# Kernel optimization log

Measured on AMD Instinct MI355X. Metric: run time of the kernel, lower is better.

The kernel has to match this reference:

```python
import jax, jax.numpy as jnp
import numpy as np

H = 400      # LSTM hidden units
K = 10       # attention window mixture components (mixtures=30 -> alpha/beta/kappa of size K)
V = 61       # vocab_size
NOUT = 121   # MDN head: 1 eos + 20*(pi, mu1, mu2, sigma1, sigma2, rho)


def setup_inputs():
    key = jax.random.key(0)
    ks = jax.random.split(key, 12)
    B, T, U = 32, 600, 64
    s = 0.05
    d = {}
    d['strokes'] = jax.random.normal(ks[0], (B, T, 3), jnp.float32)
    d['sentence'] = jax.random.uniform(ks[1], (B, U, V), dtype=jnp.float32)
    d['W1'] = jax.random.normal(ks[2], (3 + V, 4 * H), jnp.float32) * s
    d['U1r'] = jax.random.normal(ks[3], (H, 4 * H), jnp.float32) * s
    d['b1'] = jnp.zeros((4 * H,), jnp.float32)
    d['Ww'] = jax.random.normal(ks[4], (H, 3 * K), jnp.float32) * s
    d['bw'] = jnp.zeros((3 * K,), jnp.float32)
    d['W2'] = jax.random.normal(ks[5], (3 + V + H, 4 * H), jnp.float32) * s
    d['U2r'] = jax.random.normal(ks[6], (H, 4 * H), jnp.float32) * s
    d['b2'] = jnp.zeros((4 * H,), jnp.float32)
    d['W3'] = jax.random.normal(ks[7], (3 + V + H, 4 * H), jnp.float32) * s
    d['U3r'] = jax.random.normal(ks[8], (H, 4 * H), jnp.float32) * s
    d['b3'] = jnp.zeros((4 * H,), jnp.float32)
    d['Wm'] = jax.random.normal(ks[9], (3 * H, NOUT), jnp.float32) * s
    d['bm'] = jnp.zeros((NOUT,), jnp.float32)
    return d


def _lstm(x_tbd, W, Ur, b, h0, c0):
    # standard Keras-order (i, f, g, o) LSTM over time-major input [T,B,D]
    def step(carry, xt):
        h, c = carry
        z = xt @ W + h @ Ur + b
        i, f, g, o = jnp.split(z, 4, axis=-1)
        c = jax.nn.sigmoid(f) * c + jax.nn.sigmoid(i) * jnp.tanh(g)
        h = jax.nn.sigmoid(o) * jnp.tanh(c)
        return (h, c), h
    _, hs = jax.lax.scan(step, (h0, c0), x_tbd)
    return hs


def _forward(strokes, sentence, W1, U1r, b1, Ww, bw, W2, U2r, b2, W3, U3r, b3, Wm, bm):
    B, T, _ = strokes.shape
    U = sentence.shape[1]
    u_grid = jnp.arange(U, dtype=strokes.dtype)           # character positions
    x_tb = jnp.transpose(strokes, (1, 0, 2))               # [T,B,3]
    h0 = jnp.zeros((B, H), strokes.dtype)
    w0 = jnp.zeros((B, V), strokes.dtype)
    k0 = jnp.zeros((B, K), strokes.dtype)

    def step1(carry, xt):
        # Graves synthesis windowed LSTM cell: LSTM on [x_t, w_{t-1}],
        # then Gaussian-mixture soft attention over the sentence.
        h, c, w, kappa = carry
        xin = jnp.concatenate([xt, w], axis=-1)            # [B, 3+V]
        z = xin @ W1 + h @ U1r + b1
        i, f, g, o = jnp.split(z, 4, axis=-1)
        c = jax.nn.sigmoid(f) * c + jax.nn.sigmoid(i) * jnp.tanh(g)
        h = jax.nn.sigmoid(o) * jnp.tanh(c)
        p = h @ Ww + bw                                    # [B, 3K]
        alpha = jnp.exp(p[:, :K])
        beta = jnp.exp(p[:, K:2 * K])
        kappa = kappa + jnp.exp(p[:, 2 * K:])
        # phi(u) = sum_k alpha_k exp(-beta_k (kappa_k - u)^2)  -> [B,U]
        phi = jnp.einsum('bk,bku->bu', alpha,
                         jnp.exp(-beta[:, :, None] * (kappa[:, :, None] - u_grid) ** 2))
        w = jnp.einsum('bu,buv->bv', phi, sentence)        # soft window [B,V]
        return (h, c, w, kappa), jnp.concatenate([h, w], axis=-1)

    _, o1 = jax.lax.scan(step1, (h0, h0, w0, k0), x_tb)    # [T,B,H+V]
    lstm1 = o1[:, :, :H]
    win = o1[:, :, H:]
    in2 = jnp.concatenate([x_tb, win, lstm1], axis=-1)     # skip1: [T,B,3+V+H]
    lstm2 = _lstm(in2, W2, U2r, b2, h0, h0)
    in3 = jnp.concatenate([x_tb, win, lstm2], axis=-1)     # skip2
    lstm3 = _lstm(in3, W3, U3r, b3, h0, h0)
    y = jnp.concatenate([lstm1, lstm2, lstm3], axis=-1) @ Wm + bm  # [T,B,121]
    # MDN mixture coefficients
    e = jax.nn.sigmoid(y[..., 0:1])
    pi = jax.nn.softmax(y[..., 1:21], axis=-1)
    mu1 = y[..., 21:41]
    mu2 = y[..., 41:61]
    s1 = jnp.exp(y[..., 61:81])
    s2 = jnp.exp(y[..., 81:101])
    rho = jnp.tanh(y[..., 101:121])
    out = jnp.concatenate([e, pi, mu1, mu2, s1, s2, rho], axis=-1)
    return jnp.transpose(out, (1, 0, 2))                   # [B,T,121]


def reference(strokes, sentence, W1, U1r, b1, Ww, bw, W2, U2r, b2, W3, U3r, b3, Wm, bm):
    return _forward(strokes, sentence, W1, U1r, b1, Ww, bw, W2, U2r, b2, W3, U3r, b3, Wm, bm)
```

## Files before the change

### kernel.cpp

```cpp
#include <hip/hip_runtime.h>
#include <math.h>

#define T 600
#define NBLK 235

#define SEN1 256
#define SEN2 384
#define SEN3 512
#define SENB 640

#define OFF_UT1 8192
#define SZ_UT1 (1600*480)
#define OFF_UT2 (OFF_UT1 + SZ_UT1)
#define SZ_UT2 (1600*960)
#define OFF_UT3 (OFF_UT2 + SZ_UT2)
#define OFF_WWT (OFF_UT3 + SZ_UT2)
#define SZ_WWT (30*400)
#define OFF_H1 (OFF_WWT + SZ_WWT)
#define SZ_H (600*32*400)
#define OFF_H2 (OFF_H1 + SZ_H)
#define OFF_H3 (OFF_H2 + SZ_H)
#define OFF_W  (OFF_H3 + SZ_H)
#define SZ_W (600*32*61)

#define LDS_W    0
#define LDS_V    19280
#define LDS_Z    34640
#define LDS_C    35408
#define LDS_TOT  35600

__device__ __forceinline__ float sigm(float x) { return 1.f/(1.f+expf(-x)); }

#define WBAR() do { \
    asm volatile("s_waitcnt lgkmcnt(0)" ::: "memory"); \
    __builtin_amdgcn_sched_barrier(0); \
} while (0)

__global__ void init_ws(unsigned* uws) {
    for (int i = threadIdx.x + blockIdx.x*blockDim.x; i < 8192; i += blockDim.x*gridDim.x)
        uws[i] = 0u;
}

__global__ void build_ut(float* __restrict__ ws,
                         const float* __restrict__ W1, const float* __restrict__ U1r,
                         const float* __restrict__ W2, const float* __restrict__ U2r,
                         const float* __restrict__ W3, const float* __restrict__ U3r,
                         const float* __restrict__ Ww) {
    const long N1 = 1600L*480, N2 = 1600L*960;
    const long total = N1 + 2*N2 + 30L*400;
    for (long i = blockIdx.x*(long)blockDim.x + threadIdx.x; i < total;
         i += (long)gridDim.x*blockDim.x) {
        if (i < N1) {
            long c = i / 480, k = i % 480;
            float v = 0.f;
            if (k < 64) v = W1[k*1600 + c];
            else if (k < 464) v = U1r[(k-64)*1600 + c];
            ws[OFF_UT1 + c*480 + k] = v;
        } else if (i < N1 + N2) {
            long ii = i - N1; long c = ii/960, k = ii%960;
            float v = 0.f;
            if (k < 464) v = W2[k*1600 + c];
            else if (k >= 480 && k < 880) v = U2r[(k-480)*1600 + c];
            ws[OFF_UT2 + c*960 + k] = v;
        } else if (i < N1 + 2*N2) {
            long ii = i - N1 - N2; long c = ii/960, k = ii%960;
            float v = 0.f;
            if (k < 464) v = W3[k*1600 + c];
            else if (k >= 480 && k < 880) v = U3r[(k-480)*1600 + c];
            ws[OFF_UT3 + c*960 + k] = v;
        } else {
            long ii = i - N1 - 2*N2; long n = ii/400, k = ii%400;
            ws[OFF_WWT + n*400 + k] = Ww[k*30 + n];
        }
    }
}

__device__ __forceinline__ unsigned ld_cohere(const unsigned* p) {
    unsigned v;
    asm volatile("global_load_dword %0, %1, off sc0 sc1\n\t"
                 "s_waitcnt vmcnt(0)"
                 : "=v"(v) : "v"(p) : "memory");
    return v;
}
__device__ __forceinline__ void st_wt(float* p, float v) {
    asm volatile("global_store_dword %0, %1, off sc0 sc1\n\t"
                 "s_waitcnt vmcnt(0)"
                 :: "v"(p), "v"(v) : "memory");
}
__device__ __forceinline__ void st_wt_u(unsigned* p, unsigned v) {
    asm volatile("global_store_dword %0, %1, off sc0 sc1\n\t"
                 "s_waitcnt vmcnt(0)"
                 :: "v"(p), "v"(v) : "memory");
}
__device__ __forceinline__ void wait_sen(const unsigned* sen, int count,
                                         unsigned tgt, int tid) {
    if (tid < 64) {
        for (;;) {
            unsigned m = 0xFFFFFFFFu;
            for (int i = tid; i < count; i += 64) {
                unsigned v = ld_cohere(sen + i);
                m = (v < m) ? v : m;
            }
            if (__all(m >= tgt)) break;
            __builtin_amdgcn_s_sleep(1);
        }
    }
    __syncthreads();
}

template<int NQ, int KCN, int K4S, int LO, int HI>
__device__ __forceinline__ void gemm_pass(const float4* __restrict__ w4,
                                          const float4* __restrict__ v4,
                                          int lc0, int kc, int bq, int kofs4,
                                          float acc[8][4]) {
    #pragma unroll
    for (int q = 0; q < NQ; ++q) {
        int kfv = q*KCN + kc;
        if (kfv >= LO && kfv < HI) {
            int xv = kfv ^ ((kfv >> 3) & 7);
            int kfw = kofs4 + kfv;
            int xw = kfw ^ ((kfw >> 3) & 7);
            float4 va[8];
            #pragma unroll
            for (int i = 0; i < 8; ++i) va[i] = v4[(bq*8+i)*120 + xv];
            #pragma unroll
            for (int j = 0; j < 4; ++j) {
                float4 u = w4[(lc0+j)*K4S + xw];
                #pragma unroll
                for (int i = 0; i < 8; ++i)
                    acc[i][j] += va[i].x*u.x + va[i].y*u.y + va[i].z*u.z + va[i].w*u.w;
            }
        }
    }
}

__launch_bounds__(512)
__global__ void hw_main(float* __restrict__ ws,
                        const float* __restrict__ strokes, const float* __restrict__ sentence,
                        const float* __restrict__ b1, const float* __restrict__ b2,
                        const float* __restrict__ b3, const float* __restrict__ bw) {
    extern __shared__ float S[];
    const int tid = threadIdx.x;
    const int bid = blockIdx.x;
    unsigned* uws = (unsigned*)ws;
    const unsigned* sen1 = uws + SEN1;
    const unsigned* sen2 = uws + SEN2;
    const unsigned* sen3 = uws + SEN3;
    const unsigned* senB = uws + SENB;

    int role, unit0 = 0, nu = 0, L = 0, b0a = 0;
    const float* utp = nullptr; const float* biasp = nullptr; float* hout = nullptr;
    if (bid < 67)       { role = 0; L = bid;      unit0 = L*6; nu = (bid==66)?4:6; utp = ws+OFF_UT1; biasp = b1; hout = ws+OFF_H1; }
    else if (bid < 147) { role = 1; L = bid-67;   unit0 = L*5; nu = 5;             utp = ws+OFF_UT2; biasp = b2; hout = ws+OFF_H2; }
    else if (bid < 227) { role = 2; L = bid-147;  unit0 = L*5; nu = 5;             utp = ws+OFF_UT3; biasp = b3; hout = ws+OFF_H3; }
    else                { role = 3; L = bid-227;  b0a = L*4; }

    if (role <= 2) {
        const int NC = 4*nu;
        const int KCN = (role == 0) ? 20 : 24;
        const int K4S = (role == 0) ? 121 : 241;
        const int K4TOT = (role == 0) ? 120 : 240;
        const int uts = (role == 0) ? 480 : 960;
        float4* w4 = (float4*)S;
        float4* v4 = (float4*)(S + LDS_V);
        float*  vf = S + LDS_V;
        float*  z_lds = S + LDS_Z;
        float*  c_lds = S + LDS_C;

        for (int idx = tid; idx < NC*K4TOT; idx += 512) {
            int colL = idx / K4TOT, kf = idx % K4TOT;
            int gcol = (colL/nu)*400 + unit0 + (colL%nu);
            float4 val = *(const float4*)(utp + (size_t)gcol*uts + kf*4);
            w4[colL*K4S + (kf ^ ((kf>>3)&7))] = val;
        }
        for (int i = tid; i < 192; i += 512) c_lds[i] = 0.f;

        const int tile = tid / KCN, kc = tid % KCN;
        const int bq = tile / nu, cq = tile % nu;
        const bool act = (tile < 4*nu);
        float bias0 = 0.f, bias1 = 0.f;
        if (tid < 32*NC)       { int lc = tid % NC;        bias0 = biasp[(lc/nu)*400 + unit0 + (lc%nu)]; }
        if (tid + 512 < 32*NC) { int lc = (tid+512) % NC;  bias1 = biasp[(lc/nu)*400 + unit0 + (lc%nu)]; }
        const int nrole = (role == 0) ? 67 : 80;
        const unsigned* mysen = (role == 0) ? sen1 : ((role == 1) ? sen2 : sen3);
        unsigned* myword = (unsigned*)mysen + L;
        __syncthreads();

        for (int t = 0; t < T; ++t) {
            float acc[8][4];
            #pragma unroll
            for (int i = 0; i < 8; ++i)
                #pragma unroll
                for (int j = 0; j < 4; ++j) acc[i][j] = 0.f;

            if (role == 0) {
                if (t > 0) wait_sen(sen1, 67, (unsigned)t, tid);
                const float* hsrc = (t > 0) ? (ws + OFF_H1 + (size_t)(t-1)*12800) : nullptr;
                for (int idx = tid; idx < 3328; idx += 512) {
                    int b = idx/104, kf = 16 + idx%104;
                    float4 val = {0.f,0.f,0.f,0.f};
                    if (kf < 116 && hsrc) val = *(const float4*)(hsrc + b*400 + (kf*4 - 64));
                    v4[b*120 + (kf ^ ((kf>>3)&7))] = val;
                }
                __syncthreads();
                if (act) gemm_pass<6,20,121,16,116>(w4, v4, cq*4, kc, bq, 0, acc);
                if (t > 0) wait_sen(senB, 8, (unsigned)t, tid);
                const float* wsrc = (t > 0) ? (ws + OFF_W + (size_t)(t-1)*1952) : nullptr;
                {
                    int b = tid / 16, kf = tid % 16;
                    if (b < 32) {
                        float4 val;
                        if (kf == 0) {
                            const float* xp = strokes + ((size_t)b*600 + t)*3;
                            val.x = xp[0]; val.y = xp[1]; val.z = xp[2];
                            val.w = wsrc ? wsrc[b*61] : 0.f;
                        } else {
                            int k0 = kf*4 - 3;
                            if (wsrc) { val.x = wsrc[b*61+k0]; val.y = wsrc[b*61+k0+1];
                                        val.z = wsrc[b*61+k0+2]; val.w = wsrc[b*61+k0+3]; }
                            else { val.x=val.y=val.z=val.w=0.f; }
                        }
                        v4[b*120 + (kf ^ ((kf>>3)&7))] = val;
                    }
                }
                __syncthreads();
                if (act) gemm_pass<6,20,121,0,16>(w4, v4, cq*4, kc, bq, 0, acc);
            } else {
                if (role == 1) wait_sen(senB, 8, (unsigned)(t+1), tid);
                else           wait_sen(sen2, 80, (unsigned)(t+1), tid);
                const float* hsrc = ws + ((role==1)?OFF_H1:OFF_H2) + (size_t)t*12800;
                const float* wsrc = ws + OFF_W + (size_t)t*1952;
                for (int idx = tid; idx < 3840; idx += 512) {
                    int b = idx/120, kf = idx%120;
                    float4 val;
                    if (kf >= 16) {
                        if (kf < 116) val = *(const float4*)(hsrc + b*400 + (kf*4 - 64));
                        else { val.x=val.y=val.z=val.w=0.f; }
                    } else if (kf == 0) {
                        const float* xp = strokes + ((size_t)b*600 + t)*3;
                        val.x = xp[0]; val.y = xp[1]; val.z = xp[2];
                        val.w = wsrc[b*61];
                    } else {
                        int k0 = kf*4 - 3;
                        val.x = wsrc[b*61+k0]; val.y = wsrc[b*61+k0+1];
                        val.z = wsrc[b*61+k0+2]; val.w = wsrc[b*61+k0+3];
                    }
                    v4[b*120 + (kf ^ ((kf>>3)&7))] = val;
                }
                __syncthreads();
                if (act) gemm_pass<5,24,241,0,116>(w4, v4, cq*4, kc, bq, 0, acc);
                __syncthreads();
                if (t > 0) wait_sen(mysen, 80, (unsigned)t, tid);
                const float* hp2 = (t > 0) ? (ws + ((role==1)?OFF_H2:OFF_H3) + (size_t)(t-1)*12800) : nullptr;
                for (int idx = tid; idx < 3840; idx += 512) {
                    int b = idx/120, kf = idx%120;
                    float4 val = {0.f,0.f,0.f,0.f};
                    if (kf < 100 && hp2) val = *(const float4*)(hp2 + b*400 + kf*4);
                    v4[b*120 + (kf ^ ((kf>>3)&7))] = val;
                }
                __syncthreads();
                if (act) gemm_pass<5,24,241,0,100>(w4, v4, cq*4, kc, bq, 120, acc);
            }

            __syncthreads();
            const int halfk = (KCN+1)/2;
            const int SCRW = NC*32 + 4;
            const int NO = 32*NC;
            if (act && kc < halfk) {
                #pragma unroll
                for (int i = 0; i < 8; ++i) {
                    float4 w;
                    w.x=acc[i][0]; w.y=acc[i][1]; w.z=acc[i][2]; w.w=acc[i][3];
                    *(float4*)&vf[kc*SCRW + (bq*8+i)*NC + cq*4] = w;
                }
            }
            __syncthreads();
            float zs0 = 0.f, zs1 = 0.f;
            if (tid < NO)       for (int k2 = 0; k2 < halfk; ++k2) zs0 += vf[k2*SCRW + tid];
            if (tid + 512 < NO) for (int k2 = 0; k2 < halfk; ++k2) zs1 += vf[k2*SCRW + tid + 512];
            __syncthreads();
            if (act && kc >= halfk) {
                #pragma unroll
                for (int i = 0; i < 8; ++i) {
                    float4 w;
                    w.x=acc[i][0]; w.y=acc[i][1]; w.z=acc[i][2]; w.w=acc[i][3];
                    *(float4*)&vf[(kc-halfk)*SCRW + (bq*8+i)*NC + cq*4] = w;
                }
            }
            __syncthreads();
            const int rem = KCN - halfk;
            if (tid < NO) {
                for (int k2 = 0; k2 < rem; ++k2) zs0 += vf[k2*SCRW + tid];
                z_lds[tid] = zs0 + bias0;
            }
            if (tid + 512 < NO) {
                for (int k2 = 0; k2 < rem; ++k2) zs1 += vf[k2*SCRW + tid + 512];
                z_lds[tid + 512] = zs1 + bias1;
            }
            __syncthreads();
            if (tid < 32*nu) {
                int b = tid & 31, ju = tid >> 5;
                float zi = z_lds[b*NC + ju];
                float zf = z_lds[b*NC + nu + ju];
                float zg = z_lds[b*NC + 2*nu + ju];
                float zo = z_lds[b*NC + 3*nu + ju];
                float cP = c_lds[b*6 + ju];
                float cN = sigm(zf)*cP + sigm(zi)*tanhf(zg);
                float hN = sigm(zo)*tanhf(cN);
                c_lds[b*6 + ju] = cN;
                st_wt(&hout[(size_t)t*12800 + b*400 + unit0 + ju], hN);
            }
            __syncthreads();
            if (tid == 0) st_wt_u(myword, (unsigned)(t+1));
        }
    } else {
        const int wv = tid >> 6, lane = tid & 63;
        float* hb   = S;
        float* pb   = S + 1600 + (tid>>6)*32;
        float* ab   = S + 1792 + (tid>>6)*32;
        float* kap  = S + 1984 + (tid>>6)*16;
        float* phiW = S + 2112 + (tid>>6)*64;
        float* sentl= S + 2368;
        float* wwt  = S + 2368 + 15616;
        float* hbW  = hb + wv*400;
        float4* hb4 = (float4*)hbW;
        unsigned* myword = (unsigned*)senB + L;

        for (int i = tid; i < 64; i += 512) (S + 1984)[i] = 0.f;
        for (int i = tid; i < 15616; i += 512) sentl[i] = sentence[(size_t)b0a*3904 + i];
        for (int i = tid; i < 12000; i += 512) {
            int n = i/400, k = i%400;
            wwt[n*404 + k] = ws[OFF_WWT + i];
        }
        float bwv = (lane < 60 && !(lane & 1)) ? bw[lane >> 1] : 0.f;
        __syncthreads();

        for (int t = 0; t < T; ++t) {
            wait_sen(sen1, 67, (unsigned)(t+1), tid);
            if (wv < 4) {
                const float* h1t = ws + OFF_H1 + (size_t)t*12800 + (size_t)(b0a+wv)*400;
                for (int i = lane; i < 100; i += 64)
                    hb4[i] = *(const float4*)(h1t + i*4);
                WBAR();
                if (lane < 60) {
                    int n = lane >> 1, hf = lane & 1;
                    const float4* ww4 = (const float4*)(wwt + n*404) + hf*50;
                    const float4* hh4 = hb4 + hf*50;
                    float a = 0.f;
                    #pragma unroll 5
                    for (int i = 0; i < 50; ++i) {
                        float4 h = hh4[i], w = ww4[i];
                        a += h.x*w.x + h.y*w.y + h.z*w.z + h.w*w.w;
                    }
                    a += __shfl_xor(a, 1);
                    if (hf == 0) pb[n] = a + bwv;
                }
                WBAR();
                if (lane < 10) {
                    ab[lane]      = expf(pb[lane]);
                    ab[16 + lane] = expf(pb[10 + lane]);
                    kap[lane]    += expf(pb[20 + lane]);
                }
                WBAR();
                {
                    float uf = (float)lane, ph = 0.f;
                    #pragma unroll
                    for (int k0 = 0; k0 < 10; ++k0) {
                        float d = kap[k0] - uf;
                        ph += ab[k0]*expf(-ab[16 + k0]*d*d);
                    }
                    phiW[lane] = ph;
                }
                WBAR();
                if (lane < 61) {
                    const float* sp = sentl + wv*3904 + lane;
                    float wvv = 0.f;
                    #pragma unroll 4
                    for (int u = 0; u < 64; ++u) wvv += phiW[u]*sp[u*61];
                    st_wt(&ws[OFF_W + (size_t)t*1952 + (size_t)(b0a+wv)*61 + lane], wvv);
                }
            }
            __syncthreads();
            if (tid == 0) st_wt_u(myword, (unsigned)(t+1));
        }
    }
}

__launch_bounds__(256)
__global__ void out_proj(const float* __restrict__ ws, const float* __restrict__ Wm,
                         const float* __restrict__ bm, float* __restrict__ out) {
    __shared__ __align__(16) float hc[8*1200];
    __shared__ float yy[8*121];
    __shared__ float sm2[16];
    const int tid = threadIdx.x;
    const long rowbase = (long)blockIdx.x * 8;
    const float* h1h = ws + OFF_H1;
    const float* h2h = ws + OFF_H2;
    const float* h3h = ws + OFF_H3;
    for (int idx = tid; idx < 8*1200; idx += 256) {
        int i = idx/1200, k = idx%1200;
        long r = rowbase + i; int t = (int)(r >> 5), b = (int)(r & 31);
        float v;
        if (k < 400)      v = h1h[(size_t)t*12800 + b*400 + k];
        else if (k < 800) v = h2h[(size_t)t*12800 + b*400 + (k-400)];
        else              v = h3h[(size_t)t*12800 + b*400 + (k-800)];
        hc[i*1200 + k] = v;
    }
    __syncthreads();
    const int j = tid & 127, rr = tid >> 7;
    if (j < 121) {
        float a0=0.f, a1=0.f, a2=0.f, a3=0.f;
        const float* r0 = &hc[(rr*4+0)*1200];
        const float* r1 = &hc[(rr*4+1)*1200];
        const float* r2 = &hc[(rr*4+2)*1200];
        const float* r3 = &hc[(rr*4+3)*1200];
        for (int k = 0; k < 1200; ++k) {
            float wm = Wm[(size_t)k*121 + j];
            a0 += r0[k]*wm; a1 += r1[k]*wm; a2 += r2[k]*wm; a3 += r3[k]*wm;
        }
        float bb = bm[j];
        yy[(rr*4+0)*121 + j] = a0 + bb;
        yy[(rr*4+1)*121 + j] = a1 + bb;
        yy[(rr*4+2)*121 + j] = a2 + bb;
        yy[(rr*4+3)*121 + j] = a3 + bb;
    }
    __syncthreads();
    if (tid < 8) {
        const float* yr = &yy[tid*121];
        float m = yr[1];
        for (int q = 2; q < 21; ++q) m = fmaxf(m, yr[q]);
        float ssum = 0.f;
        for (int q = 1; q < 21; ++q) ssum += expf(yr[q] - m);
        sm2[tid*2] = m; sm2[tid*2+1] = ssum;
    }
    __syncthreads();
    if (j < 121) {
        for (int i2 = 0; i2 < 4; ++i2) {
            int i = rr*4 + i2;
            long r = rowbase + i; int t = (int)(r >> 5), b = (int)(r & 31);
            float y = yy[i*121 + j], o;
            if (j == 0)      o = 1.f/(1.f + expf(-y));
            else if (j < 21) o = expf(y - sm2[i*2]) / sm2[i*2+1];
            else if (j < 61) o = y;
            else if (j < 101) o = expf(y);
            else             o = tanhf(y);
            out[((size_t)b*600 + t)*121 + j] = o;
        }
    }
}

extern "C" void kernel_launch(void* const* d_in, const int* in_sizes, int n_in,
                              void* d_out, int out_size, void* d_ws, size_t ws_size,
                              hipStream_t stream) {
    const float* strokes  = (const float*)d_in[0];
    const float* sentence = (const float*)d_in[1];
    const float* W1  = (const float*)d_in[2];
    const float* U1r = (const float*)d_in[3];
    const float* b1  = (const float*)d_in[4];
    const float* Ww  = (const float*)d_in[5];
    const float* bw  = (const float*)d_in[6];
    const float* W2  = (const float*)d_in[7];
    const float* U2r = (const float*)d_in[8];
    const float* b2  = (const float*)d_in[9];
    const float* W3  = (const float*)d_in[10];
    const float* U3r = (const float*)d_in[11];
    const float* b3  = (const float*)d_in[12];
    const float* Wm  = (const float*)d_in[13];
    const float* bm  = (const float*)d_in[14];
    float* ws = (float*)d_ws;
    float* out = (float*)d_out;

    const int dyn_bytes = LDS_TOT * 4;
    (void)hipFuncSetAttribute((const void*)hw_main,
                              hipFuncAttributeMaxDynamicSharedMemorySize, dyn_bytes);

    init_ws<<<dim3(4), dim3(512), 0, stream>>>((unsigned*)ws);
    build_ut<<<dim3(1024), dim3(256), 0, stream>>>(ws, W1, U1r, W2, U2r, W3, U3r, Ww);
    hw_main<<<dim3(NBLK), dim3(512), dyn_bytes, stream>>>(ws, strokes, sentence, b1, b2, b3, bw);
    out_proj<<<dim3(2400), dim3(256), 0, stream>>>(ws, Wm, bm, out);
}
```

Measured before the change: 10.51 ms.

## Defer window/stroke input contribution of layer-1 LSTM until after the recurrent GEMM reduction

Layer-1 LSTM blocks no longer wait for the attention window before their second GEMM pass. They first run the recurrent h-part GEMM and its reduction, then wait for the window signal. The x and window contribution (64 inputs) is then computed as a small per-thread dot product against a head weight slice cached in LDS, fused into the gate nonlinearity. The aim is to take the window-block dependency off the critical path of the GEMM, at the cost of a serial 64-term dot product per output thread and extra LDS.

```diff
diff --git a/kernel.cpp b/kernel.cpp
--- a/kernel.cpp
+++ b/kernel.cpp
@@ -27,7 +27,8 @@
 #define LDS_V    19280
 #define LDS_Z    34640
 #define LDS_C    35408
-#define LDS_TOT  35600
+#define LDS_WH   35600
+#define LDS_TOT  37136
 
 __device__ __forceinline__ float sigm(float x) { return 1.f/(1.f+expf(-x)); }
 
@@ -166,6 +167,7 @@
         float*  vf = S + LDS_V;
         float*  z_lds = S + LDS_Z;
         float*  c_lds = S + LDS_C;
+        float*  whead = S + LDS_WH;
 
         for (int idx = tid; idx < NC*K4TOT; idx += 512) {
             int colL = idx / K4TOT, kf = idx % K4TOT;
@@ -174,6 +176,13 @@
             w4[colL*K4S + (kf ^ ((kf>>3)&7))] = val;
         }
         for (int i = tid; i < 192; i += 512) c_lds[i] = 0.f;
+        if (role == 0) {
+            for (int i = tid; i < 64*NC; i += 512) {
+                int k = i / NC, lc = i % NC;
+                int gcol = (lc/nu)*400 + unit0 + (lc%nu);
+                whead[i] = utp[(size_t)gcol*480 + k];
+            }
+        }
 
         const int tile = tid / KCN, kc = tid % KCN;
         const int bq = tile / nu, cq = tile % nu;
@@ -181,7 +190,6 @@
         float bias0 = 0.f, bias1 = 0.f;
         if (tid < 32*NC)       { int lc = tid % NC;        bias0 = biasp[(lc/nu)*400 + unit0 + (lc%nu)]; }
         if (tid + 512 < 32*NC) { int lc = (tid+512) % NC;  bias1 = biasp[(lc/nu)*400 + unit0 + (lc%nu)]; }
-        const int nrole = (role == 0) ? 67 : 80;
         const unsigned* mysen = (role == 0) ? sen1 : ((role == 1) ? sen2 : sen3);
         unsigned* myword = (unsigned*)mysen + L;
         __syncthreads();
@@ -196,35 +204,14 @@
             if (role == 0) {
                 if (t > 0) wait_sen(sen1, 67, (unsigned)t, tid);
                 const float* hsrc = (t > 0) ? (ws + OFF_H1 + (size_t)(t-1)*12800) : nullptr;
-                for (int idx = tid; idx < 3328; idx += 512) {
-                    int b = idx/104, kf = 16 + idx%104;
+                for (int idx = tid; idx < 3200; idx += 512) {
+                    int b = idx/100, kfi = idx%100, kf = 16 + kfi;
                     float4 val = {0.f,0.f,0.f,0.f};
-                    if (kf < 116 && hsrc) val = *(const float4*)(hsrc + b*400 + (kf*4 - 64));
+                    if (hsrc) val = *(const float4*)(hsrc + b*400 + kfi*4);
                     v4[b*120 + (kf ^ ((kf>>3)&7))] = val;
                 }
                 __syncthreads();
                 if (act) gemm_pass<6,20,121,16,116>(w4, v4, cq*4, kc, bq, 0, acc);
-                if (t > 0) wait_sen(senB, 8, (unsigned)t, tid);
-                const float* wsrc = (t > 0) ? (ws + OFF_W + (size_t)(t-1)*1952) : nullptr;
-                {
-                    int b = tid / 16, kf = tid % 16;
-                    if (b < 32) {
-                        float4 val;
-                        if (kf == 0) {
-                            const float* xp = strokes + ((size_t)b*600 + t)*3;
-                            val.x = xp[0]; val.y = xp[1]; val.z = xp[2];
-                            val.w = wsrc ? wsrc[b*61] : 0.f;
-                        } else {
-                            int k0 = kf*4 - 3;
-                            if (wsrc) { val.x = wsrc[b*61+k0]; val.y = wsrc[b*61+k0+1];
-                                        val.z = wsrc[b*61+k0+2]; val.w = wsrc[b*61+k0+3]; }
-                            else { val.x=val.y=val.z=val.w=0.f; }
-                        }
-                        v4[b*120 + (kf ^ ((kf>>3)&7))] = val;
-                    }
-                }
-                __syncthreads();
-                if (act) gemm_pass<6,20,121,0,16>(w4, v4, cq*4, kc, bq, 0, acc);
             } else {
                 if (role == 1) wait_sen(senB, 8, (unsigned)(t+1), tid);
                 else           wait_sen(sen2, 80, (unsigned)(t+1), tid);
@@ -298,17 +285,51 @@
                 z_lds[tid + 512] = zs1 + bias1;
             }
             __syncthreads();
-            if (tid < 32*nu) {
-                int b = tid & 31, ju = tid >> 5;
-                float zi = z_lds[b*NC + ju];
-                float zf = z_lds[b*NC + nu + ju];
-                float zg = z_lds[b*NC + 2*nu + ju];
-                float zo = z_lds[b*NC + 3*nu + ju];
-                float cP = c_lds[b*6 + ju];
-                float cN = sigm(zf)*cP + sigm(zi)*tanhf(zg);
-                float hN = sigm(zo)*tanhf(cN);
-                c_lds[b*6 + ju] = cN;
-                st_wt(&hout[(size_t)t*12800 + b*400 + unit0 + ju], hN);
+
+            if (role == 0) {
+                if (t > 0) wait_sen(senB, 8, (unsigned)t, tid);
+                float* wl = vf;
+                const float* wsrc = (t > 0) ? (ws + OFF_W + (size_t)(t-1)*1952) : nullptr;
+                for (int i = tid; i < 1952; i += 512) wl[i] = wsrc ? wsrc[i] : 0.f;
+                __syncthreads();
+                if (tid < 32*nu) {
+                    int b = tid & 31, ju = tid >> 5;
+                    const float* xp = strokes + ((size_t)b*600 + t)*3;
+                    float x0 = xp[0], x1 = xp[1], x2 = xp[2];
+                    const float* wb = wl + b*61;
+                    float zz[4];
+                    #pragma unroll
+                    for (int g = 0; g < 4; ++g) {
+                        int lc = g*nu + ju;
+                        float a = x0*whead[lc] + x1*whead[NC + lc] + x2*whead[2*NC + lc];
+                        const float* wh = whead + 3*NC + lc;
+                        #pragma unroll 4
+                        for (int k = 0; k < 61; ++k) a += wb[k]*wh[k*NC];
+                        zz[g] = a;
+                    }
+                    float zi = z_lds[b*NC + ju]        + zz[0];
+                    float zf = z_lds[b*NC + nu + ju]   + zz[1];
+                    float zg = z_lds[b*NC + 2*nu + ju] + zz[2];
+                    float zo = z_lds[b*NC + 3*nu + ju] + zz[3];
+                    float cP = c_lds[b*6 + ju];
+                    float cN = sigm(zf)*cP + sigm(zi)*tanhf(zg);
+                    float hN = sigm(zo)*tanhf(cN);
+                    c_lds[b*6 + ju] = cN;
+                    st_wt(&hout[(size_t)t*12800 + b*400 + unit0 + ju], hN);
+                }
+            } else {
+                if (tid < 32*nu) {
+                    int b = tid & 31, ju = tid >> 5;
+                    float zi = z_lds[b*NC + ju];
+                    float zf = z_lds[b*NC + nu + ju];
+                    float zg = z_lds[b*NC + 2*nu + ju];
+                    float zo = z_lds[b*NC + 3*nu + ju];
+                    float cP = c_lds[b*6 + ju];
+                    float cN = sigm(zf)*cP + sigm(zi)*tanhf(zg);
+                    float hN = sigm(zo)*tanhf(cN);
+                    c_lds[b*6 + ju] = cN;
+                    st_wt(&hout[(size_t)t*12800 + b*400 + unit0 + ju], hN);
+                }
             }
             __syncthreads();
             if (tid == 0) st_wt_u(myword, (unsigned)(t+1));
```

Result: slower. 13.21 ms (+25.7%).
